# Performance work log

Measured on AMD Instinct MI355X. Metric: run time of the kernel, lower is better.

Reference implementation:

```python
import jax, jax.numpy as jnp
import numpy as np

B, S, K, D, H, F = 2, 2048, 2048, 1024, 16, 4096
HD = D // H
LN_EPS = 1e-5  # nn.LayerNorm default (module's eps arg is unused by the norms)


def setup_inputs() -> dict:
    key = jax.random.key(0)
    ks = jax.random.split(key, 12)
    def w(k, shape, scale=0.02):
        return jax.random.normal(k, shape, jnp.float32) * scale
    return {
        "x": jax.random.normal(ks[0], (B, S, D), jnp.float32),
        "context": jax.random.normal(ks[1], (B, K, D), jnp.float32),
        "Wq": w(ks[2], (D, D)), "bq": jnp.zeros((D,), jnp.float32),
        "Wk": w(ks[3], (D, D)), "bk": jnp.zeros((D,), jnp.float32),
        "Wv": w(ks[4], (D, D)), "bv": jnp.zeros((D,), jnp.float32),
        "W1": w(ks[5], (F, D)), "b1": jnp.zeros((F,), jnp.float32),
        "W2": w(ks[6], (D, F)), "b2": jnp.zeros((D,), jnp.float32),
        "g1": jnp.ones((D,), jnp.float32), "be1": jnp.zeros((D,), jnp.float32),
        "g2": jnp.ones((D,), jnp.float32), "be2": jnp.zeros((D,), jnp.float32),
    }


def _ln(x, g, b):
    m = jnp.mean(x, axis=-1, keepdims=True)
    v = jnp.var(x, axis=-1, keepdims=True)
    return (x - m) / jnp.sqrt(v + LN_EPS) * g + b


def _split_heads(t, L):
    # [B, L, D] -> [B, H, L, HD]
    return t.reshape(B, L, H, HD).transpose(0, 2, 1, 3)


def reference(x, context, Wq, bq, Wk, bk, Wv, bv, W1, b1, W2, b2, g1, be1, g2, be2):
    q = _split_heads(x @ Wq.T + bq, S)
    k = _split_heads(context @ Wk.T + bk, K)
    v = _split_heads(context @ Wv.T + bv, K)
    # NOTE: original scales by sqrt(encoder_out_dim), not sqrt(head_dim)
    scores = jnp.einsum('bhqd,bhkd->bhqk', q, k) / jnp.sqrt(jnp.float32(D))
    attn = jax.nn.softmax(scores, axis=-1)
    ctx = jnp.einsum('bhqk,bhkd->bhqd', attn, v)
    # faithful to original: raw reshape of [B,H,S,HD] -> [B,S,D] (no head transpose)
    out1 = ctx.reshape(B, S, D)
    out1 = x + _ln(out1, g1, be1)
    h = jax.nn.gelu(out1 @ W1.T + b1, approximate=False)
    out2 = _ln(h @ W2.T + b2, g2, be2)
    return out1 + out2
```

## Files before the change

### kernel.cpp

```cpp
#include <hip/hip_runtime.h>
#include <hip/hip_bf16.h>

#define BB 2
#define SS 2048
#define KK 2048
#define DD 1024
#define HH 16
#define FF 4096

using bf16x8 = __attribute__((ext_vector_type(8))) __bf16;
using f32x4  = __attribute__((ext_vector_type(4))) float;
using u16 = unsigned short;

__device__ __forceinline__ float bf2f(u16 u){
  union { unsigned int i; float f; } c; c.i = ((unsigned int)u) << 16; return c.f;
}
__device__ __forceinline__ u16 f2bf(float f){
  union { float f; unsigned int i; } c; c.f = f;
  return (u16)((c.i + 0x7fffu + ((c.i >> 16) & 1u)) >> 16);
}
__device__ __forceinline__ float gelu_exact(float x){
  return 0.5f * x * (1.f + erff(x * 0.70710678118654752f));
}

__device__ __forceinline__ void gll16(const void* g, const void* l) {
  __builtin_amdgcn_global_load_lds(
      (const __attribute__((address_space(1))) void*)(unsigned long long)(size_t)g,
      (__attribute__((address_space(3))) void*)(unsigned int)(size_t)l,
      16, 0, 0);
}

#define E_X   0
#define E_CX  4194304
#define E_WQ  8388608
#define E_BQ  9437184
#define E_WK  9438208
#define E_BK  10486784
#define E_WV  10487808
#define E_BV  11536384
#define E_W1  11537408
#define E_B1  15731712
#define E_W2  15735808
#define E_B2  19930112
#define E_G1  19931136
#define E_BE1 19932160
#define E_G2  19933184
#define E_BE2 19934208
#define E_TOT 19935232

struct Ptrs { const void* p[16]; };

__global__ __launch_bounds__(256)
void convert_inputs(Ptrs ptrs, u16* __restrict__ dst)
{
  const bool is_f32 = (((const u16*)ptrs.p[12])[0] == 0);
  const int szs[16] = {4194304, 4194304, 1048576, 1024, 1048576, 1024,
                       1048576, 1024, 4194304, 4096, 4194304, 1024,
                       1024, 1024, 1024, 1024};
  long long gbase = (long long)blockIdx.x * 1024;
  int seg = 0; long long start = 0;
  while (seg < 15 && gbase >= start + szs[seg]) { start += szs[seg]; seg++; }
  const long long local = gbase - start;
  const int tid = threadIdx.x;
  u16 outv[4];
  if (is_f32) {
    const float4* s = (const float4*)((const float*)ptrs.p[seg] + local);
    float4 v = s[tid];
    outv[0] = f2bf(v.x); outv[1] = f2bf(v.y); outv[2] = f2bf(v.z); outv[3] = f2bf(v.w);
  } else {
    const uint2* s = (const uint2*)((const u16*)ptrs.p[seg] + local);
    uint2 v = s[tid];
    *(uint2*)outv = v;
  }
  *(uint2*)(dst + gbase + (long long)tid * 4) = *(uint2*)outv;
}

template<int EPI>
__device__ __forceinline__
void gemm_core(const u16* __restrict__ A, const u16* __restrict__ W,
               const u16* __restrict__ bias, u16* __restrict__ Cout,
               int M, int N, int Kd, int n0, int m0,
               u16* sA0, u16* sA1, u16* sB0, u16* sB1)
{
  const int tid = threadIdx.x;
  const int wv = tid >> 6, lane = tid & 63;
  const int wm = (wv >> 1) * 64, wn = (wv & 1) * 64;
  const int l16 = lane & 15, quad = lane >> 4;
  const int srow = tid >> 2, scol = (tid & 3) * 8;

  const u16* gA = A + (size_t)(m0 + srow) * Kd + scol;
  const u16* gB = W + (size_t)(n0 + srow) * Kd + scol;
  u16* lA0 = sA0 + wv * 512; u16* lA1 = sA1 + wv * 512;
  u16* lB0 = sB0 + wv * 512; u16* lB1 = sB1 + wv * 512;
  const size_t rs = (size_t)64 * Kd;

  f32x4 acc[4][4] = {};

  auto mma_step = [&](const u16* sA, const u16* sB) {
    bf16x8 af[4], wf[4];
#pragma unroll
    for (int i = 0; i < 4; i++)
      af[i] = *(const bf16x8*)(sA + (wm + 16 * i + l16) * 32 + quad * 8);
#pragma unroll
    for (int j = 0; j < 4; j++)
      wf[j] = *(const bf16x8*)(sB + (wn + 16 * j + l16) * 32 + quad * 8);
#pragma unroll
    for (int i = 0; i < 4; i++)
#pragma unroll
      for (int j = 0; j < 4; j++)
        acc[i][j] = __builtin_amdgcn_mfma_f32_16x16x32_bf16(af[i], wf[j], acc[i][j], 0, 0, 0);
  };

  gll16(gA, lA0); gll16(gA + rs, lA0 + 2048);
  gll16(gB, lB0); gll16(gB + rs, lB0 + 2048);

  for (int k0 = 0; k0 < Kd; k0 += 64) {
    __syncthreads();
    gll16(gA + k0 + 32, lA1); gll16(gA + rs + k0 + 32, lA1 + 2048);
    gll16(gB + k0 + 32, lB1); gll16(gB + rs + k0 + 32, lB1 + 2048);
    mma_step(sA0, sB0);
    __syncthreads();
    if (k0 + 64 < Kd) {
      gll16(gA + k0 + 64, lA0); gll16(gA + rs + k0 + 64, lA0 + 2048);
      gll16(gB + k0 + 64, lB0); gll16(gB + rs + k0 + 64, lB0 + 2048);
    }
    mma_step(sA1, sB1);
  }

#pragma unroll
  for (int i = 0; i < 4; i++)
#pragma unroll
    for (int j = 0; j < 4; j++) {
      const int mb = m0 + wm + 16 * i + quad * 4;
      const int n  = n0 + wn + 16 * j + l16;
      const float bv = bf2f(bias[n]);
      if (EPI == 3) {
        u16 pk[4];
#pragma unroll
        for (int r = 0; r < 4; r++) pk[r] = f2bf(acc[i][j][r] + bv);
        const int b = mb >> 11, key = mb & 2047;
        *(uint2*)(Cout + ((size_t)((b * HH + (n >> 6)) * 64 + (n & 63))) * KK + key)
            = *(uint2*)pk;
      } else {
#pragma unroll
        for (int r = 0; r < 4; r++) {
          float vv = acc[i][j][r] + bv;
          if (EPI == 1) vv = gelu_exact(vv);
          Cout[(size_t)(mb + r) * N + n] = f2bf(vv);
        }
      }
    }
}

template<int EPI>
__global__ __launch_bounds__(256, 2)
void gemm_bt(const u16* __restrict__ A, const u16* __restrict__ W,
             const u16* __restrict__ bias, u16* __restrict__ Cout,
             int M, int N, int Kd)
{
  __shared__ u16 sA0[4096], sA1[4096], sB0[4096], sB1[4096];
  gemm_core<EPI>(A, W, bias, Cout, M, N, Kd,
                 blockIdx.x * 128, blockIdx.y * 128, sA0, sA1, sB0, sB1);
}

__global__ __launch_bounds__(256, 2)
void qkv_gemm(const u16* __restrict__ conv, u16* __restrict__ q_ws,
              u16* __restrict__ k_ws, u16* __restrict__ vt_ws)
{
  __shared__ u16 sA0[4096], sA1[4096], sB0[4096], sB1[4096];
  const int n0 = blockIdx.x * 128, m0 = blockIdx.y * 128;
  const int z = blockIdx.z;
  if (z == 0)
    gemm_core<0>(conv + E_X,  conv + E_WQ, conv + E_BQ, q_ws,  BB*SS, DD, DD, n0, m0, sA0, sA1, sB0, sB1);
  else if (z == 1)
    gemm_core<0>(conv + E_CX, conv + E_WK, conv + E_BK, k_ws,  BB*KK, DD, DD, n0, m0, sA0, sA1, sB0, sB1);
  else
    gemm_core<3>(conv + E_CX, conv + E_WV, conv + E_BV, vt_ws, BB*KK, DD, DD, n0, m0, sA0, sA1, sB0, sB1);
}

#define ATT_SCALE 0.03125f

__global__ __launch_bounds__(256, 2)
void attn_flash(const u16* __restrict__ q, const u16* __restrict__ k,
                const u16* __restrict__ vt, u16* __restrict__ ctx)
{
  __shared__ u16 Qs[128 * 64];
  __shared__ u16 Ks0[64 * 64], Ks1[64 * 64], Vt0[64 * 64], Vt1[64 * 64];
  __shared__ u16 Ps[4][32 * 72];
  const int tid = threadIdx.x, wv = tid >> 6, lane = tid & 63;
  const int l16 = lane & 15, quad = lane >> 4;
  const int s0 = blockIdx.x * 128;
  const int bh = blockIdx.y, b = bh >> 4, h = bh & 15;
  const size_t qgbase = ((size_t)b * SS + s0) * DD + h * 64;
  const size_t kgbase = (size_t)b * KK * DD + h * 64;
  const size_t vtbase = (size_t)bh * 64 * KK;
  const int srow = tid >> 3, sc8 = tid & 7;

  auto stage_kv = [&](u16* Ks, u16* Vt, int kt) {
#pragma unroll
    for (int n = 0; n < 2; n++) {
      int row = srow + 32 * n, c8 = sc8 ^ (row & 7);
      gll16(k + kgbase + (size_t)(kt + row) * DD + c8 * 8, Ks + (n * 256 + wv * 64) * 8);
      gll16(vt + vtbase + (size_t)row * KK + kt + c8 * 8, Vt + (n * 256 + wv * 64) * 8);
    }
  };

#pragma unroll
  for (int n = 0; n < 4; n++) {
    int row = srow + 32 * n, c8 = sc8 ^ (row & 7);
    gll16(q + qgbase + (size_t)row * DD + c8 * 8, Qs + (n * 256 + wv * 64) * 8);
  }
  stage_kv(Ks0, Vt0, 0);
  __syncthreads();

  bf16x8 qf[2][2];
#pragma unroll
  for (int mi = 0; mi < 2; mi++)
#pragma unroll
    for (int kc = 0; kc < 2; kc++)
      qf[mi][kc] = *(const bf16x8*)(Qs + (wv * 32 + mi * 16 + l16) * 64
                                    + (((kc << 2) | quad) ^ (l16 & 7)) * 8);

  f32x4 O[2][4] = {};
  float psum[2] = {0.f, 0.f};
  u16* Psw = Ps[wv];

  auto compute = [&](const u16* Ks, const u16* Vt) {
#pragma unroll
    for (int mi = 0; mi < 2; mi++) {
      uint2 pk2[4];
#pragma unroll
      for (int jj = 0; jj < 4; jj++) {
        f32x4 c = {};
#pragma unroll
        for (int kc = 0; kc < 2; kc++) {
          bf16x8 ak = *(const bf16x8*)(Ks + (jj * 16 + l16) * 64
                                       + (((kc << 2) | quad) ^ (l16 & 7)) * 8);
          c = __builtin_amdgcn_mfma_f32_16x16x32_bf16(ak, qf[mi][kc], c, 0, 0, 0);
        }
        float p0 = __expf(c[0] * ATT_SCALE);
        float p1 = __expf(c[1] * ATT_SCALE);
        float p2 = __expf(c[2] * ATT_SCALE);
        float p3 = __expf(c[3] * ATT_SCALE);
        psum[mi] += (p0 + p1) + (p2 + p3);
        union { float f; unsigned u; } u0{p0}, u1{p1}, u2{p2}, u3{p3};
        pk2[jj].x = __builtin_amdgcn_perm(u1.u, u0.u, 0x07060302u);
        pk2[jj].y = __builtin_amdgcn_perm(u3.u, u2.u, 0x07060302u);
      }
#pragma unroll
      for (int jj = 0; jj < 4; jj++)
        *(uint2*)(Psw + (mi * 16 + l16) * 72 + jj * 16 + quad * 4) = pk2[jj];
    }
    asm volatile("s_waitcnt lgkmcnt(0)" ::: "memory");
    bf16x8 pf[2][2];
#pragma unroll
    for (int mi = 0; mi < 2; mi++)
#pragma unroll
      for (int kc = 0; kc < 2; kc++)
        pf[mi][kc] = *(const bf16x8*)(Psw + (mi * 16 + l16) * 72 + kc * 32 + quad * 8);
#pragma unroll
    for (int mi = 0; mi < 2; mi++)
#pragma unroll
      for (int db = 0; db < 4; db++)
#pragma unroll
        for (int kc = 0; kc < 2; kc++) {
          bf16x8 bv = *(const bf16x8*)(Vt + (db * 16 + l16) * 64
                                       + (((kc << 2) | quad) ^ (l16 & 7)) * 8);
          O[mi][db] = __builtin_amdgcn_mfma_f32_16x16x32_bf16(pf[mi][kc], bv, O[mi][db], 0, 0, 0);
        }
  };

  for (int kt = 0; kt < KK; kt += 128) {
    __syncthreads();
    stage_kv(Ks1, Vt1, kt + 64);
    compute(Ks0, Vt0);
    __syncthreads();
    if (kt + 128 < KK) stage_kv(Ks0, Vt0, kt + 128);
    compute(Ks1, Vt1);
  }

  float lf[2];
#pragma unroll
  for (int mi = 0; mi < 2; mi++) {
    float t = psum[mi];
    t += __shfl_xor(t, 16, 64);
    t += __shfl_xor(t, 32, 64);
    lf[mi] = t;
  }
#pragma unroll
  for (int mi = 0; mi < 2; mi++)
#pragma unroll
    for (int r = 0; r < 4; r++) {
      float lv = __shfl(lf[mi], quad * 4 + r, 64);
      float inv = 1.f / lv;
      int qrow = s0 + wv * 32 + mi * 16 + quad * 4 + r;
#pragma unroll
      for (int db = 0; db < 4; db++)
        ctx[((size_t)bh * SS + qrow) * 64 + db * 16 + l16] = f2bf(O[mi][db][r] * inv);
    }
}

__global__ __launch_bounds__(256)
void ln1_res(const u16* __restrict__ src, const u16* __restrict__ x,
             const u16* __restrict__ g, const u16* __restrict__ be,
             u16* __restrict__ out_bf)
{
  const int row = blockIdx.x, tid = threadIdx.x;
  const size_t base = (size_t)row * 1024;
  float vv[4]; float s = 0.f, s2 = 0.f;
#pragma unroll
  for (int i = 0; i < 4; i++) {
    vv[i] = bf2f(src[base + tid + 256 * i]);
    s += vv[i]; s2 += vv[i] * vv[i];
  }
#pragma unroll
  for (int off = 32; off; off >>= 1) { s += __shfl_xor(s, off, 64); s2 += __shfl_xor(s2, off, 64); }
  __shared__ float red[2][4];
  const int wave = tid >> 6, lane = tid & 63;
  if (lane == 0) { red[0][wave] = s; red[1][wave] = s2; }
  __syncthreads();
  s  = red[0][0] + red[0][1] + red[0][2] + red[0][3];
  s2 = red[1][0] + red[1][1] + red[1][2] + red[1][3];
  const float mean = s * (1.f / 1024.f);
  const float rstd = rsqrtf(s2 * (1.f / 1024.f) - mean * mean + 1e-5f);
#pragma unroll
  for (int i = 0; i < 4; i++) {
    int col = tid + 256 * i;
    float nv = (vv[i] - mean) * rstd * bf2f(g[col]) + bf2f(be[col]);
    out_bf[base + col] = f2bf(bf2f(x[base + col]) + nv);
  }
}

__global__ __launch_bounds__(256)
void ln2_res(const u16* __restrict__ lin2, const u16* __restrict__ o1,
             const u16* __restrict__ g, const u16* __restrict__ be,
             const void* __restrict__ detect, void* __restrict__ out)
{
  const bool f32out = (((const u16*)detect)[0] == 0);
  const int row = blockIdx.x, tid = threadIdx.x;
  const size_t base = (size_t)row * 1024;
  float vv[4]; float s = 0.f, s2 = 0.f;
#pragma unroll
  for (int i = 0; i < 4; i++) {
    vv[i] = bf2f(lin2[base + tid + 256 * i]);
    s += vv[i]; s2 += vv[i] * vv[i];
  }
#pragma unroll
  for (int off = 32; off; off >>= 1) { s += __shfl_xor(s, off, 64); s2 += __shfl_xor(s2, off, 64); }
  __shared__ float red[2][4];
  const int wave = tid >> 6, lane = tid & 63;
  if (lane == 0) { red[0][wave] = s; red[1][wave] = s2; }
  __syncthreads();
  s  = red[0][0] + red[0][1] + red[0][2] + red[0][3];
  s2 = red[1][0] + red[1][1] + red[1][2] + red[1][3];
  const float mean = s * (1.f / 1024.f);
  const float rstd = rsqrtf(s2 * (1.f / 1024.f) - mean * mean + 1e-5f);
#pragma unroll
  for (int i = 0; i < 4; i++) {
    int col = tid + 256 * i;
    float nv = (vv[i] - mean) * rstd * bf2f(g[col]) + bf2f(be[col]);
    float res = bf2f(o1[base + col]) + nv;
    if (f32out) ((float*)out)[base + col] = res;
    else        ((u16*)out)[base + col]  = f2bf(res);
  }
}

extern "C" void kernel_launch(void* const* d_in, const int* in_sizes, int n_in,
                              void* d_out, int out_size, void* d_ws, size_t ws_size,
                              hipStream_t stream)
{
  char* ws = (char*)d_ws;
  const size_t MB = 1024 * 1024;
  u16* conv   = (u16*)ws;
  u16* q_ws   = (u16*)(ws + 40 * MB);
  u16* k_ws   = (u16*)(ws + 48 * MB);
  u16* vt_ws  = (u16*)(ws + 56 * MB);
  u16* ctx_ws = (u16*)(ws + 64 * MB);
  u16* o1_bf  = (u16*)(ws + 72 * MB);
  u16* h_ws   = (u16*)(ws + 80 * MB);
  u16* lin2_ws = q_ws;

  Ptrs ptrs;
  for (int i = 0; i < 16; i++) ptrs.p[i] = d_in[i];

  dim3 blk(256);
  const int M = BB * SS;

  convert_inputs<<<dim3(E_TOT / 1024), blk, 0, stream>>>(ptrs, conv);

  qkv_gemm<<<dim3(DD / 128, M / 128, 3), blk, 0, stream>>>(conv, q_ws, k_ws, vt_ws);

  attn_flash<<<dim3(SS / 128, BB * HH), blk, 0, stream>>>(q_ws, k_ws, vt_ws, ctx_ws);

  ln1_res<<<dim3(M), blk, 0, stream>>>(ctx_ws, conv + E_X, conv + E_G1, conv + E_BE1, o1_bf);

  gemm_bt<1><<<dim3(FF / 128, M / 128), blk, 0, stream>>>(o1_bf, conv + E_W1, conv + E_B1, h_ws, M, FF, DD);
  gemm_bt<0><<<dim3(DD / 128, M / 128), blk, 0, stream>>>(h_ws, conv + E_W2, conv + E_B2, lin2_ws, M, DD, FF);

  ln2_res<<<dim3(M), blk, 0, stream>>>(lin2_ws, o1_bf, conv + E_G2, conv + E_BE2, d_in[12], d_out);
}
```

Measured before the change: 345.2 us.

## Deepen GEMM LDS pipeline to 4 stages with swizzle; single-buffer attention for occupancy

The GEMM core moves from a 2-stage double buffer to a 4-stage ring of LDS buffers. It waits with explicit vmcnt/lgkmcnt and a raw s_barrier, and XOR-swizzles the 32-wide rows to cut LDS bank conflicts. The attention kernel drops its K/V double buffering in favour of a single buffer and raises the launch bound to 3 blocks per CU, trading load/compute overlap for occupancy. The GEMM now uses twice the LDS, 64KB per block, which may limit its own occupancy.

```diff
diff --git a/kernel.cpp b/kernel.cpp
--- a/kernel.cpp
+++ b/kernel.cpp
@@ -80,51 +80,59 @@
 void gemm_core(const u16* __restrict__ A, const u16* __restrict__ W,
                const u16* __restrict__ bias, u16* __restrict__ Cout,
                int M, int N, int Kd, int n0, int m0,
-               u16* sA0, u16* sA1, u16* sB0, u16* sB1)
+               u16* sA, u16* sB)
 {
   const int tid = threadIdx.x;
   const int wv = tid >> 6, lane = tid & 63;
   const int wm = (wv >> 1) * 64, wn = (wv & 1) * 64;
   const int l16 = lane & 15, quad = lane >> 4;
-  const int srow = tid >> 2, scol = (tid & 3) * 8;
+  const int srow = tid >> 2;
+  const int scol = ((tid & 3) ^ ((srow >> 1) & 3)) * 8;
 
   const u16* gA = A + (size_t)(m0 + srow) * Kd + scol;
   const u16* gB = W + (size_t)(n0 + srow) * Kd + scol;
-  u16* lA0 = sA0 + wv * 512; u16* lA1 = sA1 + wv * 512;
-  u16* lB0 = sB0 + wv * 512; u16* lB1 = sB1 + wv * 512;
   const size_t rs = (size_t)64 * Kd;
 
+  auto issueAB = [&](int stage, int k) {
+    u16* lA = sA + stage * 4096 + wv * 512;
+    u16* lB = sB + stage * 4096 + wv * 512;
+    gll16(gA + k, lA); gll16(gA + rs + k, lA + 2048);
+    gll16(gB + k, lB); gll16(gB + rs + k, lB + 2048);
+  };
+
   f32x4 acc[4][4] = {};
 
-  auto mma_step = [&](const u16* sA, const u16* sB) {
-    bf16x8 af[4], wf[4];
-#pragma unroll
-    for (int i = 0; i < 4; i++)
-      af[i] = *(const bf16x8*)(sA + (wm + 16 * i + l16) * 32 + quad * 8);
-#pragma unroll
-    for (int j = 0; j < 4; j++)
-      wf[j] = *(const bf16x8*)(sB + (wn + 16 * j + l16) * 32 + quad * 8);
-#pragma unroll
-    for (int i = 0; i < 4; i++)
-#pragma unroll
-      for (int j = 0; j < 4; j++)
-        acc[i][j] = __builtin_amdgcn_mfma_f32_16x16x32_bf16(af[i], wf[j], acc[i][j], 0, 0, 0);
-  };
-
-  gll16(gA, lA0); gll16(gA + rs, lA0 + 2048);
-  gll16(gB, lB0); gll16(gB + rs, lB0 + 2048);
-
-  for (int k0 = 0; k0 < Kd; k0 += 64) {
-    __syncthreads();
-    gll16(gA + k0 + 32, lA1); gll16(gA + rs + k0 + 32, lA1 + 2048);
-    gll16(gB + k0 + 32, lB1); gll16(gB + rs + k0 + 32, lB1 + 2048);
-    mma_step(sA0, sB0);
-    __syncthreads();
-    if (k0 + 64 < Kd) {
-      gll16(gA + k0 + 64, lA0); gll16(gA + rs + k0 + 64, lA0 + 2048);
-      gll16(gB + k0 + 64, lB0); gll16(gB + rs + k0 + 64, lB0 + 2048);
+  issueAB(0, 0); issueAB(1, 32); issueAB(2, 64);
+
+  const int P = Kd >> 5;
+  for (int p = 0; p < P; p += 4) {
+#pragma unroll
+    for (int s = 0; s < 4; s++) {
+      const int pp = p + s;
+      asm volatile("s_waitcnt vmcnt(8) lgkmcnt(0)" ::: "memory");
+      asm volatile("s_barrier" ::: "memory");
+      const int kn = (pp + 3 < P) ? (pp + 3) * 32 : (P - 1) * 32;
+      issueAB((pp + 3) & 3, kn);
+
+      const u16* cA = sA + s * 4096;
+      const u16* cB = sB + s * 4096;
+      bf16x8 af[4], wf[4];
+#pragma unroll
+      for (int i = 0; i < 4; i++) {
+        const int row = wm + 16 * i + l16;
+        af[i] = *(const bf16x8*)(cA + row * 32 + (quad ^ ((row >> 1) & 3)) * 8);
+      }
+#pragma unroll
+      for (int j = 0; j < 4; j++) {
+        const int row = wn + 16 * j + l16;
+        wf[j] = *(const bf16x8*)(cB + row * 32 + (quad ^ ((row >> 1) & 3)) * 8);
+      }
+#pragma unroll
+      for (int i = 0; i < 4; i++)
+#pragma unroll
+        for (int j = 0; j < 4; j++)
+          acc[i][j] = __builtin_amdgcn_mfma_f32_16x16x32_bf16(af[i], wf[j], acc[i][j], 0, 0, 0);
     }
-    mma_step(sA1, sB1);
   }
 
 #pragma unroll
@@ -133,7 +141,7 @@
     for (int j = 0; j < 4; j++) {
       const int mb = m0 + wm + 16 * i + quad * 4;
       const int n  = n0 + wn + 16 * j + l16;
-      const float bv = bf2f(bias[n]);
+      const float bv = bf2f(*(volatile const u16*)(bias + n));
       if (EPI == 3) {
         u16 pk[4];
 #pragma unroll
@@ -158,34 +166,36 @@
              const u16* __restrict__ bias, u16* __restrict__ Cout,
              int M, int N, int Kd)
 {
-  __shared__ u16 sA0[4096], sA1[4096], sB0[4096], sB1[4096];
+  __shared__ u16 sA[4 * 4096];
+  __shared__ u16 sB[4 * 4096];
   gemm_core<EPI>(A, W, bias, Cout, M, N, Kd,
-                 blockIdx.x * 128, blockIdx.y * 128, sA0, sA1, sB0, sB1);
+                 blockIdx.x * 128, blockIdx.y * 128, sA, sB);
 }
 
 __global__ __launch_bounds__(256, 2)
 void qkv_gemm(const u16* __restrict__ conv, u16* __restrict__ q_ws,
               u16* __restrict__ k_ws, u16* __restrict__ vt_ws)
 {
-  __shared__ u16 sA0[4096], sA1[4096], sB0[4096], sB1[4096];
+  __shared__ u16 sA[4 * 4096];
+  __shared__ u16 sB[4 * 4096];
   const int n0 = blockIdx.x * 128, m0 = blockIdx.y * 128;
   const int z = blockIdx.z;
   if (z == 0)
-    gemm_core<0>(conv + E_X,  conv + E_WQ, conv + E_BQ, q_ws,  BB*SS, DD, DD, n0, m0, sA0, sA1, sB0, sB1);
+    gemm_core<0>(conv + E_X,  conv + E_WQ, conv + E_BQ, q_ws,  BB*SS, DD, DD, n0, m0, sA, sB);
   else if (z == 1)
-    gemm_core<0>(conv + E_CX, conv + E_WK, conv + E_BK, k_ws,  BB*KK, DD, DD, n0, m0, sA0, sA1, sB0, sB1);
+    gemm_core<0>(conv + E_CX, conv + E_WK, conv + E_BK, k_ws,  BB*KK, DD, DD, n0, m0, sA, sB);
   else
-    gemm_core<3>(conv + E_CX, conv + E_WV, conv + E_BV, vt_ws, BB*KK, DD, DD, n0, m0, sA0, sA1, sB0, sB1);
+    gemm_core<3>(conv + E_CX, conv + E_WV, conv + E_BV, vt_ws, BB*KK, DD, DD, n0, m0, sA, sB);
 }
 
 #define ATT_SCALE 0.03125f
 
-__global__ __launch_bounds__(256, 2)
+__global__ __launch_bounds__(256, 3)
 void attn_flash(const u16* __restrict__ q, const u16* __restrict__ k,
                 const u16* __restrict__ vt, u16* __restrict__ ctx)
 {
   __shared__ u16 Qs[128 * 64];
-  __shared__ u16 Ks0[64 * 64], Ks1[64 * 64], Vt0[64 * 64], Vt1[64 * 64];
+  __shared__ u16 Ks[64 * 64], Vt[64 * 64];
   __shared__ u16 Ps[4][32 * 72];
   const int tid = threadIdx.x, wv = tid >> 6, lane = tid & 63;
   const int l16 = lane & 15, quad = lane >> 4;
@@ -196,36 +206,35 @@
   const size_t vtbase = (size_t)bh * 64 * KK;
   const int srow = tid >> 3, sc8 = tid & 7;
 
-  auto stage_kv = [&](u16* Ks, u16* Vt, int kt) {
+#pragma unroll
+  for (int n = 0; n < 4; n++) {
+    int row = srow + 32 * n, c8 = sc8 ^ (row & 7);
+    gll16(q + qgbase + (size_t)row * DD + c8 * 8, Qs + (n * 256 + wv * 64) * 8);
+  }
+  __syncthreads();
+
+  bf16x8 qf[2][2];
+#pragma unroll
+  for (int mi = 0; mi < 2; mi++)
+#pragma unroll
+    for (int kc = 0; kc < 2; kc++)
+      qf[mi][kc] = *(const bf16x8*)(Qs + (wv * 32 + mi * 16 + l16) * 64
+                                    + (((kc << 2) | quad) ^ (l16 & 7)) * 8);
+
+  f32x4 O[2][4] = {};
+  float psum[2] = {0.f, 0.f};
+  u16* Psw = Ps[wv];
+
+  for (int kt = 0; kt < KK; kt += 64) {
+    __syncthreads();
 #pragma unroll
     for (int n = 0; n < 2; n++) {
       int row = srow + 32 * n, c8 = sc8 ^ (row & 7);
       gll16(k + kgbase + (size_t)(kt + row) * DD + c8 * 8, Ks + (n * 256 + wv * 64) * 8);
       gll16(vt + vtbase + (size_t)row * KK + kt + c8 * 8, Vt + (n * 256 + wv * 64) * 8);
     }
-  };
-
-#pragma unroll
-  for (int n = 0; n < 4; n++) {
-    int row = srow + 32 * n, c8 = sc8 ^ (row & 7);
-    gll16(q + qgbase + (size_t)row * DD + c8 * 8, Qs + (n * 256 + wv * 64) * 8);
-  }
-  stage_kv(Ks0, Vt0, 0);
-  __syncthreads();
-
-  bf16x8 qf[2][2];
-#pragma unroll
-  for (int mi = 0; mi < 2; mi++)
-#pragma unroll
-    for (int kc = 0; kc < 2; kc++)
-      qf[mi][kc] = *(const bf16x8*)(Qs + (wv * 32 + mi * 16 + l16) * 64
-                                    + (((kc << 2) | quad) ^ (l16 & 7)) * 8);
-
-  f32x4 O[2][4] = {};
-  float psum[2] = {0.f, 0.f};
-  u16* Psw = Ps[wv];
-
-  auto compute = [&](const u16* Ks, const u16* Vt) {
+    __syncthreads();
+
 #pragma unroll
     for (int mi = 0; mi < 2; mi++) {
       uint2 pk2[4];
@@ -268,15 +277,6 @@
                                        + (((kc << 2) | quad) ^ (l16 & 7)) * 8);
           O[mi][db] = __builtin_amdgcn_mfma_f32_16x16x32_bf16(pf[mi][kc], bv, O[mi][db], 0, 0, 0);
         }
-  };
-
-  for (int kt = 0; kt < KK; kt += 128) {
-    __syncthreads();
-    stage_kv(Ks1, Vt1, kt + 64);
-    compute(Ks0, Vt0);
-    __syncthreads();
-    if (kt + 128 < KK) stage_kv(Ks0, Vt0, kt + 128);
-    compute(Ks1, Vt1);
   }
 
   float lf[2];
```

After: 368.3 us. 6.7% more time.
